# Optimization experiments

Measured on AMD Instinct MI355X. Metric: run time of the kernel, lower is better.

The kernel has to match this reference:

```python
import math
import jax, jax.numpy as jnp
import numpy as np

B, T, IN_DIM = 8, 2048, 256
HEAD_TOTAL = 256  # out_dim * n_heads
NEG = -1e9


def make_mask(t):
    # torch: tril(ones, diagonal=-1).bool() -> masked_fill(-1e9)
    # i.e., entry (i, j) is -1e9 when j < i (anti-causal), 0 otherwise.
    i = jnp.arange(t)[:, None]
    j = jnp.arange(t)[None, :]
    return jnp.where(j < i, jnp.float32(NEG), jnp.float32(0.0))  # [T, T]


def setup_inputs() -> dict:
    key = jax.random.key(0)
    kx, kq, kk = jax.random.split(key, 3)
    x = jax.random.normal(kx, (B, T, IN_DIM), dtype=jnp.float32)
    # nn.Linear weights are [out_features, in_features]
    s = 1.0 / math.sqrt(IN_DIM)
    Wq = jax.random.uniform(kq, (HEAD_TOTAL, IN_DIM), dtype=jnp.float32, minval=-s, maxval=s)
    Wk = jax.random.uniform(kk, (HEAD_TOTAL, IN_DIM), dtype=jnp.float32, minval=-s, maxval=s)
    return {"x": x, "Wq": Wq, "Wk": Wk}


def reference(x, Wq, Wk):
    # q, k: [B, T, HEAD_TOTAL]
    q = jnp.einsum('bti,oi->bto', x, Wq)
    k = jnp.einsum('bsi,oi->bso', x, Wk)
    scale = 1.0 / math.sqrt(x.shape[-1])  # sqrt(in_dim), as in the source
    mask = make_mask(x.shape[1])
    # e: [B, T, T] masked pre-softmax scores (what the torch forward computes)
    e = jnp.einsum('bto,bso->bts', q, k) * scale + mask
    return e
```

## Files before the change

kernel.cpp:

```cpp
#include <hip/hip_runtime.h>
#include <hip/hip_bf16.h>
#include <stdint.h>

#define B_DIM 8
#define T_DIM 2048
#define INNER 256
#define NEGV (-1e9f)
#define SCALE 0.0625f

typedef __bf16 bf16_t;
typedef __bf16 bf16x8 __attribute__((ext_vector_type(8)));
typedef float f32x4 __attribute__((ext_vector_type(4)));

__device__ inline void gload_lds16(const bf16_t* g, bf16_t* lds) {
  __builtin_amdgcn_global_load_lds(
      (__attribute__((address_space(1))) void*)(g),
      (__attribute__((address_space(3))) void*)(lds),
      16, 0, 0);
}

__device__ inline void stage_tile(const bf16_t* gbase, int ldg,
                                  bf16_t (*lds)[64], int tid) {
  const int l = tid & 63;
  const int w = tid >> 6;
  const int sub = l >> 3;
  const int ce = (l & 7) * 8;
#pragma unroll
  for (int i = 0; i < 4; ++i) {
    const int chunk = i * 4 + w;
    const int row = chunk * 8 + sub;
    gload_lds16(gbase + (size_t)row * ldg + ce, &lds[chunk * 8][0]);
  }
}

__device__ inline void stage_tile_cvt(const float* gbase, int ldg,
                                      bf16_t (*lds)[64], int tid) {
  const int l = tid & 63;
  const int w = tid >> 6;
  const int sub = l >> 3;
  const int ce = (l & 7) * 8;
  f32x4 v[4][2];
#pragma unroll
  for (int i = 0; i < 4; ++i) {
    const int row = (i * 4 + w) * 8 + sub;
    const float* p = gbase + (size_t)row * ldg + ce;
    v[i][0] = *(const f32x4*)p;
    v[i][1] = *(const f32x4*)(p + 4);
  }
#pragma unroll
  for (int i = 0; i < 4; ++i) {
    const int row = (i * 4 + w) * 8 + sub;
    bf16x8 o;
#pragma unroll
    for (int j = 0; j < 4; ++j) {
      o[j]     = (bf16_t)v[i][0][j];
      o[4 + j] = (bf16_t)v[i][1][j];
    }
    *(bf16x8*)&lds[row][ce] = o;
  }
}

template <int KDIM>
__device__ inline void gemm_bt_128(const bf16_t* A, const bf16_t* Bm, int ld,
                                   bf16_t (*Al)[64], bf16_t (*Bl)[64],
                                   f32x4 acc[4][4], int tid) {
  const int l = tid & 63;
  const int wid = tid >> 6;
  const int wr = wid >> 1, wc = wid & 1;
  const int lr = l & 15;
  const int kg = l >> 4;
#pragma unroll
  for (int k0 = 0; k0 < KDIM; k0 += 64) {
    stage_tile(A + k0, ld, Al, tid);
    stage_tile(Bm + k0, ld, Bl, tid);
    __syncthreads();
#pragma unroll
    for (int kk = 0; kk < 2; ++kk) {
      bf16x8 af[4], bfm[4];
#pragma unroll
      for (int f = 0; f < 4; ++f) {
        af[f]  = *(const bf16x8*)&Al[wr * 64 + f * 16 + lr][kk * 32 + kg * 8];
        bfm[f] = *(const bf16x8*)&Bl[wc * 64 + f * 16 + lr][kk * 32 + kg * 8];
      }
#pragma unroll
      for (int m = 0; m < 4; ++m)
#pragma unroll
        for (int n = 0; n < 4; ++n)
          acc[m][n] = __builtin_amdgcn_mfma_f32_16x16x32_bf16(
              af[m], bfm[n], acc[m][n], 0, 0, 0);
    }
    __syncthreads();
  }
}

__global__ __launch_bounds__(256) void proj_kernel(
    const float* __restrict__ x, const float* __restrict__ Wq,
    const float* __restrict__ Wk, bf16_t* __restrict__ Q,
    bf16_t* __restrict__ Kout) {
  __shared__ bf16_t Al[128][64];
  __shared__ bf16_t Bl[128][64];
  const int tid = threadIdx.x;
  const int mrow = blockIdx.x * 128;
  const int ncol = blockIdx.y * 128;
  const float* W = blockIdx.z ? Wk : Wq;
  bf16_t* O = blockIdx.z ? Kout : Q;

  const int l = tid & 63, wid = tid >> 6, wr = wid >> 1, wc = wid & 1;
  const int lr = l & 15, kg = l >> 4;

  f32x4 acc[4][4] = {};
  const float* Ax = x + (size_t)mrow * INNER;
  const float* Bw = W + (size_t)ncol * INNER;
#pragma unroll
  for (int k0 = 0; k0 < INNER; k0 += 64) {
    stage_tile_cvt(Ax + k0, INNER, Al, tid);
    stage_tile_cvt(Bw + k0, INNER, Bl, tid);
    __syncthreads();
#pragma unroll
    for (int kk = 0; kk < 2; ++kk) {
      bf16x8 af[4], bfm[4];
#pragma unroll
      for (int f = 0; f < 4; ++f) {
        af[f]  = *(const bf16x8*)&Al[wr * 64 + f * 16 + lr][kk * 32 + kg * 8];
        bfm[f] = *(const bf16x8*)&Bl[wc * 64 + f * 16 + lr][kk * 32 + kg * 8];
      }
#pragma unroll
      for (int m = 0; m < 4; ++m)
#pragma unroll
        for (int n = 0; n < 4; ++n)
          acc[m][n] = __builtin_amdgcn_mfma_f32_16x16x32_bf16(
              af[m], bfm[n], acc[m][n], 0, 0, 0);
    }
    __syncthreads();
  }

#pragma unroll
  for (int m = 0; m < 4; ++m)
#pragma unroll
    for (int n = 0; n < 4; ++n)
#pragma unroll
      for (int j = 0; j < 4; ++j) {
        int r = mrow + wr * 64 + m * 16 + kg * 4 + j;
        int c = ncol + wc * 64 + n * 16 + lr;
        O[(size_t)r * INNER + c] = (bf16_t)acc[m][n][j];
      }
}

__global__ __launch_bounds__(256) void scores_kernel(
    const bf16_t* __restrict__ Q, const bf16_t* __restrict__ Kin,
    float* __restrict__ E) {
  const int bid = blockIdx.x;
  const int b = bid & 7;
  const int lid = bid >> 3;
  const int rt = lid >> 4;
  const int ct = lid & 15;
  const int tid = threadIdx.x;
  float* Eb = E + (size_t)b * T_DIM * T_DIM;
  const int trow = rt * 128, scol = ct * 128;

  if (ct < rt) {
    const f32x4 neg = {NEGV, NEGV, NEGV, NEGV};
#pragma unroll
    for (int it = 0; it < 16; ++it) {
      int idx = it * 256 + tid;
      int r = idx >> 5, c4 = idx & 31;
      *(f32x4*)&Eb[(size_t)(trow + r) * T_DIM + scol + c4 * 4] = neg;
    }
    return;
  }

  __shared__ bf16_t Al[128][64];
  __shared__ bf16_t Bl[128][64];
  f32x4 acc[4][4] = {};
  const bf16_t* Qb = Q + (size_t)b * T_DIM * INNER;
  const bf16_t* Kb = Kin + (size_t)b * T_DIM * INNER;
  gemm_bt_128<INNER>(Qb + (size_t)trow * INNER, Kb + (size_t)scol * INNER,
                     INNER, Al, Bl, acc, tid);

  const int l = tid & 63, wid = tid >> 6, wr = wid >> 1, wc = wid & 1;
  const int lr = l & 15, kg = l >> 4;
  const bool diag = (ct == rt);
#pragma unroll
  for (int m = 0; m < 4; ++m)
#pragma unroll
    for (int n = 0; n < 4; ++n)
#pragma unroll
      for (int j = 0; j < 4; ++j) {
        int t = trow + wr * 64 + m * 16 + kg * 4 + j;
        int s = scol + wc * 64 + n * 16 + lr;
        float v = acc[m][n][j] * SCALE;
        if (diag && s < t) v += NEGV;
        Eb[(size_t)t * T_DIM + s] = v;
      }
}

extern "C" void kernel_launch(void* const* d_in, const int* in_sizes, int n_in,
                              void* d_out, int out_size, void* d_ws,
                              size_t ws_size, hipStream_t stream) {
  const float* x  = (const float*)d_in[0];
  const float* Wq = (const float*)d_in[1];
  const float* Wk = (const float*)d_in[2];
  float* out = (float*)d_out;

  const size_t n_x = (size_t)B_DIM * T_DIM * INNER;

  bf16_t* Q = (bf16_t*)d_ws;
  bf16_t* K = Q + n_x;

  dim3 g1(B_DIM * T_DIM / 128, INNER / 128, 2);
  proj_kernel<<<g1, dim3(256), 0, stream>>>(x, Wq, Wk, Q, K);

  scores_kernel<<<2048, 256, 0, stream>>>(Q, K, out);
}
```

Measured before the change: 47.08 us.

## Fold Wq and Wk into one matrix and project x once

Rewrites the scores as x·(Wq^T Wk)·x^T. A small kernel computes the 256x256 combined matrix in fp32 and stores it as bf16, then one projection GEMM produces Y = x·M, and the scores kernel multiplies Y by x, which it converts from fp32 on the fly. This halves the projection GEMM work and the bf16 workspace writes. In exchange the scores kernel now reads fp32 x and converts it instead of loading bf16 K, and an extra tiny launch is added. Rounding the combined matrix to bf16 also changes the numerics slightly.

```diff
diff --git a/kernel.cpp b/kernel.cpp
--- a/kernel.cpp
+++ b/kernel.cpp
@@ -60,61 +60,45 @@
   }
 }
 
-template <int KDIM>
-__device__ inline void gemm_bt_128(const bf16_t* A, const bf16_t* Bm, int ld,
-                                   bf16_t (*Al)[64], bf16_t (*Bl)[64],
-                                   f32x4 acc[4][4], int tid) {
-  const int l = tid & 63;
-  const int wid = tid >> 6;
-  const int wr = wid >> 1, wc = wid & 1;
-  const int lr = l & 15;
-  const int kg = l >> 4;
-#pragma unroll
-  for (int k0 = 0; k0 < KDIM; k0 += 64) {
-    stage_tile(A + k0, ld, Al, tid);
-    stage_tile(Bm + k0, ld, Bl, tid);
-    __syncthreads();
-#pragma unroll
-    for (int kk = 0; kk < 2; ++kk) {
-      bf16x8 af[4], bfm[4];
-#pragma unroll
-      for (int f = 0; f < 4; ++f) {
-        af[f]  = *(const bf16x8*)&Al[wr * 64 + f * 16 + lr][kk * 32 + kg * 8];
-        bfm[f] = *(const bf16x8*)&Bl[wc * 64 + f * 16 + lr][kk * 32 + kg * 8];
-      }
-#pragma unroll
-      for (int m = 0; m < 4; ++m)
-#pragma unroll
-        for (int n = 0; n < 4; ++n)
-          acc[m][n] = __builtin_amdgcn_mfma_f32_16x16x32_bf16(
-              af[m], bfm[n], acc[m][n], 0, 0, 0);
-    }
-    __syncthreads();
-  }
-}
-
-__global__ __launch_bounds__(256) void proj_kernel(
-    const float* __restrict__ x, const float* __restrict__ Wq,
-    const float* __restrict__ Wk, bf16_t* __restrict__ Q,
-    bf16_t* __restrict__ Kout) {
+__global__ __launch_bounds__(256) void m_kernel(
+    const float* __restrict__ Wq, const float* __restrict__ Wk,
+    bf16_t* __restrict__ BT) {
+  const int j = blockIdx.x;
+  const int i = threadIdx.x;
+  float a0 = 0.f, a1 = 0.f, a2 = 0.f, a3 = 0.f;
+#pragma unroll 8
+  for (int o = 0; o < INNER; o += 4) {
+    const float k0 = Wk[(size_t)(o + 0) * INNER + j];
+    const float k1 = Wk[(size_t)(o + 1) * INNER + j];
+    const float k2 = Wk[(size_t)(o + 2) * INNER + j];
+    const float k3 = Wk[(size_t)(o + 3) * INNER + j];
+    a0 += Wq[(size_t)(o + 0) * INNER + i] * k0;
+    a1 += Wq[(size_t)(o + 1) * INNER + i] * k1;
+    a2 += Wq[(size_t)(o + 2) * INNER + i] * k2;
+    a3 += Wq[(size_t)(o + 3) * INNER + i] * k3;
+  }
+  BT[(size_t)j * INNER + i] = (bf16_t)((a0 + a1) + (a2 + a3));
+}
+
+__global__ __launch_bounds__(256) void y_kernel(
+    const float* __restrict__ x, const bf16_t* __restrict__ BT,
+    bf16_t* __restrict__ Y) {
   __shared__ bf16_t Al[128][64];
   __shared__ bf16_t Bl[128][64];
   const int tid = threadIdx.x;
   const int mrow = blockIdx.x * 128;
   const int ncol = blockIdx.y * 128;
-  const float* W = blockIdx.z ? Wk : Wq;
-  bf16_t* O = blockIdx.z ? Kout : Q;
 
   const int l = tid & 63, wid = tid >> 6, wr = wid >> 1, wc = wid & 1;
   const int lr = l & 15, kg = l >> 4;
 
   f32x4 acc[4][4] = {};
   const float* Ax = x + (size_t)mrow * INNER;
-  const float* Bw = W + (size_t)ncol * INNER;
+  const bf16_t* Bb = BT + (size_t)ncol * INNER;
 #pragma unroll
   for (int k0 = 0; k0 < INNER; k0 += 64) {
     stage_tile_cvt(Ax + k0, INNER, Al, tid);
-    stage_tile_cvt(Bw + k0, INNER, Bl, tid);
+    stage_tile(Bb + k0, INNER, Bl, tid);
     __syncthreads();
 #pragma unroll
     for (int kk = 0; kk < 2; ++kk) {
@@ -142,12 +126,12 @@
       for (int j = 0; j < 4; ++j) {
         int r = mrow + wr * 64 + m * 16 + kg * 4 + j;
         int c = ncol + wc * 64 + n * 16 + lr;
-        O[(size_t)r * INNER + c] = (bf16_t)acc[m][n][j];
+        Y[(size_t)r * INNER + c] = (bf16_t)acc[m][n][j];
       }
 }
 
 __global__ __launch_bounds__(256) void scores_kernel(
-    const bf16_t* __restrict__ Q, const bf16_t* __restrict__ Kin,
+    const bf16_t* __restrict__ Y, const float* __restrict__ x,
     float* __restrict__ E) {
   const int bid = blockIdx.x;
   const int b = bid & 7;
@@ -171,14 +155,35 @@
 
   __shared__ bf16_t Al[128][64];
   __shared__ bf16_t Bl[128][64];
-  f32x4 acc[4][4] = {};
-  const bf16_t* Qb = Q + (size_t)b * T_DIM * INNER;
-  const bf16_t* Kb = Kin + (size_t)b * T_DIM * INNER;
-  gemm_bt_128<INNER>(Qb + (size_t)trow * INNER, Kb + (size_t)scol * INNER,
-                     INNER, Al, Bl, acc, tid);
-
   const int l = tid & 63, wid = tid >> 6, wr = wid >> 1, wc = wid & 1;
   const int lr = l & 15, kg = l >> 4;
+
+  f32x4 acc[4][4] = {};
+  const bf16_t* Ya = Y + ((size_t)b * T_DIM + trow) * INNER;
+  const float* xs = x + ((size_t)b * T_DIM + scol) * INNER;
+#pragma unroll
+  for (int k0 = 0; k0 < INNER; k0 += 64) {
+    stage_tile(Ya + k0, INNER, Al, tid);
+    stage_tile_cvt(xs + k0, INNER, Bl, tid);
+    __syncthreads();
+#pragma unroll
+    for (int kk = 0; kk < 2; ++kk) {
+      bf16x8 af[4], bfm[4];
+#pragma unroll
+      for (int f = 0; f < 4; ++f) {
+        af[f]  = *(const bf16x8*)&Al[wr * 64 + f * 16 + lr][kk * 32 + kg * 8];
+        bfm[f] = *(const bf16x8*)&Bl[wc * 64 + f * 16 + lr][kk * 32 + kg * 8];
+      }
+#pragma unroll
+      for (int m = 0; m < 4; ++m)
+#pragma unroll
+        for (int n = 0; n < 4; ++n)
+          acc[m][n] = __builtin_amdgcn_mfma_f32_16x16x32_bf16(
+              af[m], bfm[n], acc[m][n], 0, 0, 0);
+    }
+    __syncthreads();
+  }
+
   const bool diag = (ct == rt);
 #pragma unroll
   for (int m = 0; m < 4; ++m)
@@ -204,11 +209,13 @@
 
   const size_t n_x = (size_t)B_DIM * T_DIM * INNER;
 
-  bf16_t* Q = (bf16_t*)d_ws;
-  bf16_t* K = Q + n_x;
-
-  dim3 g1(B_DIM * T_DIM / 128, INNER / 128, 2);
-  proj_kernel<<<g1, dim3(256), 0, stream>>>(x, Wq, Wk, Q, K);
-
-  scores_kernel<<<2048, 256, 0, stream>>>(Q, K, out);
-}
+  bf16_t* Y  = (bf16_t*)d_ws;
+  bf16_t* BT = Y + n_x;
+
+  m_kernel<<<256, 256, 0, stream>>>(Wq, Wk, BT);
+
+  dim3 g1(B_DIM * T_DIM / 128, INNER / 128);
+  y_kernel<<<g1, dim3(256), 0, stream>>>(x, BT, Y);
+
+  scores_kernel<<<2048, 256, 0, stream>>>(Y, x, out);
+}
```

Result: slower. 62.56 us (+32.9%).
